# Kernel optimization log

Measured on AMD Instinct MI355X. Metric: run time of the kernel, lower is better.

Reference implementation:

```python
import jax, jax.numpy as jnp
import numpy as np


def setup_inputs() -> dict:
    key = jax.random.key(0)
    k1, k2, k3, k4 = jax.random.split(key, 4)
    B, IN, OUT, S = 8192, 2048, 3072, 8
    scale = 1.0 / (IN ** 0.5)
    x = jax.random.normal(k1, (B, IN), dtype=jnp.float32)
    subject_ids = jax.random.randint(k2, (B,), 0, S, dtype=jnp.int64)
    weights = jax.random.normal(k3, (S, IN, OUT), dtype=jnp.float32) * scale
    bias = jax.random.normal(k4, (S, OUT), dtype=jnp.float32) * scale
    return {"x": x, "subject_ids": subject_ids, "weights": weights, "bias": bias}


def reference(x, subject_ids, weights, bias):
    # Math: out[b] = x[b] @ weights[subject_ids[b]] + bias[subject_ids[b]]
    # Avoid materializing the [B, in, out] gathered weight tensor:
    # contract via a one-hot subject selector instead (same math).
    S = weights.shape[0]
    onehot = jax.nn.one_hot(subject_ids, S, dtype=x.dtype)  # [B, S]
    # [B,d] x [S,d,o] x [B,S] -> [B,o]; intermediate is at most [B,S,o]
    out = jnp.einsum('bd,sdo,bs->bo', x, weights, onehot)
    out = out + bias[subject_ids]  # [B, out]
    return out
```

## Files before the change

### kernel.cpp

```cpp
#include <hip/hip_runtime.h>
#include <hip/hip_bf16.h>
#include <stdint.h>

#define B_ROWS 8192
#define K_DIM  2048
#define N_DIM  3072
#define S_NUM  8

#define BM 128
#define BN 128
#define BK 32
#define NK (K_DIM / BK)
#define MAX_TILES 72

#define LDA 40
#define LDB 40

typedef __bf16 bf16x8 __attribute__((ext_vector_type(8)));
typedef float  f32x4  __attribute__((ext_vector_type(4)));
typedef unsigned int   u32x4 __attribute__((ext_vector_type(4)));
typedef unsigned short u16x8 __attribute__((ext_vector_type(8)));

#define WS_CNT    0
#define WS_OFFS   256
#define WS_TILES  512
#define WS_TILEM  1024
#define WS_RANK   4096
#define WS_PERM   36864
#define WS_XPERM  262144
#define WS_WT     34603008
#define WS_NEED   135266304ULL

__device__ __forceinline__ unsigned int f2bf_pk(float lo, float hi) {
#if __has_builtin(__builtin_amdgcn_cvt_pk_bf16_f32)
    typedef __bf16 bf16x2_t __attribute__((ext_vector_type(2)));
    bf16x2_t v = __builtin_amdgcn_cvt_pk_bf16_f32(lo, hi);
    return __builtin_bit_cast(unsigned int, v);
#else
    unsigned int a = __builtin_bit_cast(unsigned int, lo);
    unsigned int b = __builtin_bit_cast(unsigned int, hi);
    a += 0x7FFFu + ((a >> 16) & 1u);
    b += 0x7FFFu + ((b >> 16) & 1u);
    return (a >> 16) | (b & 0xFFFF0000u);
#endif
}

__device__ __forceinline__ void gl_lds16(const void* g, void* l) {
    __builtin_amdgcn_global_load_lds(
        (const __attribute__((address_space(1))) void*)g,
        (__attribute__((address_space(3))) void*)l, 16, 0, 0);
}

__global__ void zero_cnt_kernel(int* __restrict__ cnt) {
    if (threadIdx.x < S_NUM) cnt[threadIdx.x] = 0;
}

__global__ void bucket_kernel(const int* __restrict__ ids,
                              int* __restrict__ cnt,
                              unsigned short* __restrict__ perm,
                              int* __restrict__ rank) {
    const int b = blockIdx.x * blockDim.x + threadIdx.x;
    const int lane = threadIdx.x & 63;
    const int s = ids[b];
    #pragma unroll
    for (int sub = 0; sub < S_NUM; ++sub) {
        unsigned long long m = __ballot(s == sub);
        if (s == sub) {
            int prefix = __popcll(m & ((1ull << lane) - 1ull));
            int leader = __ffsll((unsigned long long)m) - 1;
            int base = 0;
            if (lane == leader) base = atomicAdd(&cnt[sub], __popcll(m));
            base = __shfl(base, leader);
            perm[sub * B_ROWS + base + prefix] = (unsigned short)b;
            rank[b] = base + prefix;
        }
    }
}

__global__ void plan_kernel(const int* __restrict__ cnt, int* __restrict__ offs,
                            int* __restrict__ tile_s, int* __restrict__ tile_m) {
    if (threadIdx.x == 0 && blockIdx.x == 0) {
        int t = 0, o = 0;
        for (int s = 0; s < S_NUM; ++s) {
            offs[s] = o; o += cnt[s];
            for (int m0 = 0; m0 < cnt[s]; m0 += BM) {
                tile_s[t] = s; tile_m[t] = m0; ++t;
            }
        }
        for (; t < MAX_TILES; ++t) { tile_s[t] = -1; tile_m[t] = 0; }
    }
}

__global__ void convert_x_kernel(const float* __restrict__ x,
                                 const int* __restrict__ ids,
                                 const int* __restrict__ rank,
                                 const int* __restrict__ offs,
                                 unsigned short* __restrict__ xq) {
    const int b = blockIdx.x;
    const int dst = offs[ids[b]] + rank[b];
    const float* src = x + (size_t)b * K_DIM + threadIdx.x * 8;
    f32x4 v0 = *(const f32x4*)(src + 0);
    f32x4 v1 = *(const f32x4*)(src + 4);
    u32x4 p = { f2bf_pk(v0[0], v0[1]), f2bf_pk(v0[2], v0[3]),
                f2bf_pk(v1[0], v1[1]), f2bf_pk(v1[2], v1[3]) };
    *(u32x4*)(xq + (size_t)dst * K_DIM + threadIdx.x * 8) = p;
}

#define TW_LD 136
__global__ void convert_w_kernel(const float* __restrict__ w,
                                 unsigned short* __restrict__ wt) {
    const int kt = blockIdx.x, nt = blockIdx.y, s = blockIdx.z;
    __shared__ __align__(16) unsigned short lds[32 * TW_LD];

    const int tid = threadIdx.x;
    {
        const int k = tid >> 3;
        const int nseg = tid & 7;
        const float* src = w + ((size_t)s * K_DIM + kt * 32 + k) * N_DIM
                             + nt * 128 + nseg * 16;
        f32x4 v0 = *(const f32x4*)(src + 0);
        f32x4 v1 = *(const f32x4*)(src + 4);
        f32x4 v2 = *(const f32x4*)(src + 8);
        f32x4 v3 = *(const f32x4*)(src + 12);
        u32x4 p0 = { f2bf_pk(v0[0], v0[1]), f2bf_pk(v0[2], v0[3]),
                     f2bf_pk(v1[0], v1[1]), f2bf_pk(v1[2], v1[3]) };
        u32x4 p1 = { f2bf_pk(v2[0], v2[1]), f2bf_pk(v2[2], v2[3]),
                     f2bf_pk(v3[0], v3[1]), f2bf_pk(v3[2], v3[3]) };
        *(u32x4*)&lds[k * TW_LD + nseg * 16 + 0] = p0;
        *(u32x4*)&lds[k * TW_LD + nseg * 16 + 8] = p1;
    }
    __syncthreads();
    {
        const int n = tid >> 1;
        const int half = tid & 1;
        u16x8 o0, o1;
        #pragma unroll
        for (int j = 0; j < 8; ++j) {
            o0[j] = lds[(half * 16 + j) * TW_LD + n];
            o1[j] = lds[(half * 16 + 8 + j) * TW_LD + n];
        }
        unsigned short* dst = wt + ((size_t)s * N_DIM + nt * 128 + n) * K_DIM
                                 + kt * 32 + half * 16;
        *(u16x8*)(dst + 0) = o0;
        *(u16x8*)(dst + 8) = o1;
    }
}

__global__ __launch_bounds__(256, 4)
void gemm_bf16_kernel(const unsigned short* __restrict__ xq,
                      const unsigned short* __restrict__ wt,
                      const float* __restrict__ bias,
                      const int* __restrict__ cnt,
                      const int* __restrict__ offs,
                      const int* __restrict__ tile_s,
                      const int* __restrict__ tile_m,
                      const unsigned short* __restrict__ perm,
                      float* __restrict__ out) {
    const int s = tile_s[blockIdx.x];
    if (s < 0) return;
    const int row0 = tile_m[blockIdx.x];
    const int rows = min(BM, cnt[s] - row0);
    const int n0   = blockIdx.y * BN;

    __shared__ __align__(16) unsigned short sA[BM * BK];
    __shared__ __align__(16) unsigned short sB[BN * BK];
    __shared__ int prow[BM];

    const int tid = threadIdx.x;
    if (tid < BM) {
        int rr = (tid < rows) ? tid : (rows - 1);
        prow[tid] = (int)perm[s * B_ROWS + row0 + rr];
    }

    const int lane = tid & 63;
    const int wid  = tid >> 6;
    const int rsub = lane >> 2;
    const int seg  = lane & 3;

    const unsigned short* ag0 = xq + ((size_t)(offs[s] + row0 + wid * 32 + rsub)) * K_DIM + seg * 8;
    const unsigned short* ag1 = ag0 + (size_t)16 * K_DIM;
    const unsigned short* bg0 = wt + ((size_t)s * N_DIM + n0 + wid * 32 + rsub) * K_DIM + seg * 8;
    const unsigned short* bg1 = bg0 + (size_t)16 * K_DIM;
    unsigned short* al0 = &sA[(wid * 32) * BK];
    unsigned short* al1 = &sA[(wid * 32 + 16) * BK];
    unsigned short* bl0 = &sB[(wid * 32) * BK];
    unsigned short* bl1 = &sB[(wid * 32 + 16) * BK];

    const int wm  = (wid >> 1) * 64;
    const int wn  = (wid & 1) * 64;
    const int l15 = lane & 15;
    const int quad = lane >> 4;

    f32x4 acc[4][4] = {};

    for (int ks = 0; ks < NK; ++ks) {
        gl_lds16(ag0, al0);
        gl_lds16(ag1, al1);
        gl_lds16(bg0, bl0);
        gl_lds16(bg1, bl1);
        __syncthreads();

        bf16x8 af[4], bfr[4];
        #pragma unroll
        for (int mt = 0; mt < 4; ++mt)
            af[mt] = *(const bf16x8*)&sA[(wm + mt * 16 + l15) * BK + quad * 8];
        #pragma unroll
        for (int nt = 0; nt < 4; ++nt)
            bfr[nt] = *(const bf16x8*)&sB[(wn + nt * 16 + l15) * BK + quad * 8];

        #pragma unroll
        for (int mt = 0; mt < 4; ++mt)
            #pragma unroll
            for (int nt = 0; nt < 4; ++nt)
                acc[mt][nt] = __builtin_amdgcn_mfma_f32_16x16x32_bf16(
                    af[mt], bfr[nt], acc[mt][nt], 0, 0, 0);

        __syncthreads();
        ag0 += BK; ag1 += BK; bg0 += BK; bg1 += BK;
    }

    float bvals[4];
    #pragma unroll
    for (int nt = 0; nt < 4; ++nt)
        bvals[nt] = bias[s * N_DIM + n0 + wn + nt * 16 + l15];

    #pragma unroll
    for (int mt = 0; mt < 4; ++mt) {
        #pragma unroll
        for (int r = 0; r < 4; ++r) {
            int rl = wm + mt * 16 + quad * 4 + r;
            if (rl < rows) {
                float* op = out + (size_t)prow[rl] * N_DIM + n0 + wn + l15;
                #pragma unroll
                for (int nt = 0; nt < 4; ++nt)
                    op[nt * 16] = acc[mt][nt][r] + bvals[nt];
            }
        }
    }
}

__global__ __launch_bounds__(256, 3)
void subject_gemm_fb(const float* __restrict__ x,
                     const float* __restrict__ w,
                     const float* __restrict__ bias,
                     const int* __restrict__ cnt,
                     const int* __restrict__ tile_s,
                     const int* __restrict__ tile_m,
                     const unsigned short* __restrict__ perm,
                     float* __restrict__ out) {
    const int s = tile_s[blockIdx.x];
    if (s < 0) return;
    const int row0 = tile_m[blockIdx.x];
    const int rows = min(BM, cnt[s] - row0);
    const int n0   = blockIdx.y * BN;

    __shared__ __align__(16) unsigned short sA[BM * LDA];
    __shared__ __align__(16) unsigned short sB[BN * LDB];
    __shared__ int prow[BM];

    const int tid = threadIdx.x;
    if (tid < BM) {
        int rr = (tid < rows) ? tid : (rows - 1);
        prow[tid] = (int)perm[s * B_ROWS + row0 + rr];
    }
    __syncthreads();

    const int ar = tid >> 1;
    const int ah = tid & 1;
    const float* xp = x + (size_t)prow[ar] * K_DIM + ah * 16;
    const int bn  = tid & 127;
    const int bk2 = tid >> 7;
    const float* wp = w + (size_t)s * ((size_t)K_DIM * N_DIM)
                        + (size_t)(bk2 * 16) * N_DIM + (n0 + bn);

    const int lane = tid & 63;
    const int wid  = tid >> 6;
    const int wm   = (wid >> 1) * 64;
    const int wn   = (wid & 1) * 64;
    const int l15  = lane & 15;
    const int quad = lane >> 4;

    f32x4 acc[4][4] = {};
    f32x4 a0, a1, a2, a3;
    float bv[16];
    {
        a0 = *(const f32x4*)(xp + 0);  a1 = *(const f32x4*)(xp + 4);
        a2 = *(const f32x4*)(xp + 8);  a3 = *(const f32x4*)(xp + 12);
        #pragma unroll
        for (int i = 0; i < 16; ++i) bv[i] = wp[(size_t)i * N_DIM];
    }

    for (int ks = 0; ks < NK; ++ks) {
        u32x4 pa0 = { f2bf_pk(a0[0],a0[1]), f2bf_pk(a0[2],a0[3]),
                      f2bf_pk(a1[0],a1[1]), f2bf_pk(a1[2],a1[3]) };
        u32x4 pa1 = { f2bf_pk(a2[0],a2[1]), f2bf_pk(a2[2],a2[3]),
                      f2bf_pk(a3[0],a3[1]), f2bf_pk(a3[2],a3[3]) };
        u32x4 pb0 = { f2bf_pk(bv[0],bv[1]),   f2bf_pk(bv[2],bv[3]),
                      f2bf_pk(bv[4],bv[5]),   f2bf_pk(bv[6],bv[7]) };
        u32x4 pb1 = { f2bf_pk(bv[8],bv[9]),   f2bf_pk(bv[10],bv[11]),
                      f2bf_pk(bv[12],bv[13]), f2bf_pk(bv[14],bv[15]) };

        __syncthreads();
        *(u32x4*)&sA[ar * LDA + ah * 16 + 0] = pa0;
        *(u32x4*)&sA[ar * LDA + ah * 16 + 8] = pa1;
        *(u32x4*)&sB[bn * LDB + bk2 * 16 + 0] = pb0;
        *(u32x4*)&sB[bn * LDB + bk2 * 16 + 8] = pb1;
        __syncthreads();

        if (ks + 1 < NK) {
            const float* xq2 = xp + (ks + 1) * BK;
            a0 = *(const f32x4*)(xq2 + 0);  a1 = *(const f32x4*)(xq2 + 4);
            a2 = *(const f32x4*)(xq2 + 8);  a3 = *(const f32x4*)(xq2 + 12);
            const float* wq = wp + (size_t)((ks + 1) * BK) * N_DIM;
            #pragma unroll
            for (int i = 0; i < 16; ++i) bv[i] = wq[(size_t)i * N_DIM];
        }

        bf16x8 af[4], bfr[4];
        #pragma unroll
        for (int mt = 0; mt < 4; ++mt)
            af[mt] = *(const bf16x8*)&sA[(wm + mt * 16 + l15) * LDA + quad * 8];
        #pragma unroll
        for (int nt = 0; nt < 4; ++nt)
            bfr[nt] = *(const bf16x8*)&sB[(wn + nt * 16 + l15) * LDB + quad * 8];

        #pragma unroll
        for (int mt = 0; mt < 4; ++mt)
            #pragma unroll
            for (int nt = 0; nt < 4; ++nt)
                acc[mt][nt] = __builtin_amdgcn_mfma_f32_16x16x32_bf16(
                    af[mt], bfr[nt], acc[mt][nt], 0, 0, 0);
    }

    float bvals[4];
    #pragma unroll
    for (int nt = 0; nt < 4; ++nt)
        bvals[nt] = bias[s * N_DIM + n0 + wn + nt * 16 + l15];
    #pragma unroll
    for (int mt = 0; mt < 4; ++mt) {
        #pragma unroll
        for (int r = 0; r < 4; ++r) {
            int rl = wm + mt * 16 + quad * 4 + r;
            if (rl < rows) {
                float* op = out + (size_t)prow[rl] * N_DIM + n0 + wn + l15;
                #pragma unroll
                for (int nt = 0; nt < 4; ++nt)
                    op[nt * 16] = acc[mt][nt][r] + bvals[nt];
            }
        }
    }
}

extern "C" void kernel_launch(void* const* d_in, const int* in_sizes, int n_in,
                              void* d_out, int out_size, void* d_ws, size_t ws_size,
                              hipStream_t stream) {
    const float* x    = (const float*)d_in[0];
    const int*   sid  = (const int*)d_in[1];
    const float* w    = (const float*)d_in[2];
    const float* bias = (const float*)d_in[3];
    float* out = (float*)d_out;

    char* ws = (char*)d_ws;
    int* cnt    = (int*)(ws + WS_CNT);
    int* offs   = (int*)(ws + WS_OFFS);
    int* tile_s = (int*)(ws + WS_TILES);
    int* tile_m = (int*)(ws + WS_TILEM);
    int* rank   = (int*)(ws + WS_RANK);
    unsigned short* perm = (unsigned short*)(ws + WS_PERM);

    hipLaunchKernelGGL(zero_cnt_kernel, dim3(1), dim3(64), 0, stream, cnt);
    hipLaunchKernelGGL(bucket_kernel, dim3(B_ROWS / 256), dim3(256), 0, stream,
                       sid, cnt, perm, rank);
    hipLaunchKernelGGL(plan_kernel, dim3(1), dim3(64), 0, stream,
                       cnt, offs, tile_s, tile_m);

    if (ws_size >= WS_NEED) {
        unsigned short* xq = (unsigned short*)(ws + WS_XPERM);
        unsigned short* wt = (unsigned short*)(ws + WS_WT);
        hipLaunchKernelGGL(convert_x_kernel, dim3(B_ROWS), dim3(256), 0, stream,
                           x, sid, rank, offs, xq);
        hipLaunchKernelGGL(convert_w_kernel, dim3(K_DIM / 32, N_DIM / 128, S_NUM),
                           dim3(256), 0, stream, w, wt);
        dim3 grid(MAX_TILES, N_DIM / BN);
        hipLaunchKernelGGL(gemm_bf16_kernel, grid, dim3(256), 0, stream,
                           xq, wt, bias, cnt, offs, tile_s, tile_m, perm, out);
    } else {
        dim3 grid(MAX_TILES, N_DIM / BN);
        hipLaunchKernelGGL(subject_gemm_fb, grid, dim3(256), 0, stream,
                           x, w, bias, cnt, tile_s, tile_m, perm, out);
    }
}
```

Measured before the change: 556.3 us.

## Replace bf16 GEMM with 256x256 double-buffered, XOR-swizzled, ping-pong scheduled kernel

```diff
diff --git a/kernel.cpp b/kernel.cpp
--- a/kernel.cpp
+++ b/kernel.cpp
@@ -7,12 +7,17 @@
 #define N_DIM  3072
 #define S_NUM  8
 
-#define BM 128
-#define BN 128
-#define BK 32
-#define NK (K_DIM / BK)
+#define BM 256
+#define BN 256
+#define BK 64
+#define NT (K_DIM / BK)
+#define MAX_T256 40
+
+#define BMF 128
+#define BNF 128
+#define BKF 32
+#define NKF (K_DIM / BKF)
 #define MAX_TILES 72
-
 #define LDA 40
 #define LDB 40
 
@@ -23,13 +28,15 @@
 
 #define WS_CNT    0
 #define WS_OFFS   256
-#define WS_TILES  512
-#define WS_TILEM  1024
+#define WS_T256S  512
+#define WS_T256M  768
+#define WS_TILES  1024
+#define WS_TILEM  1536
 #define WS_RANK   4096
 #define WS_PERM   36864
 #define WS_XPERM  262144
-#define WS_WT     34603008
-#define WS_NEED   135266304ULL
+#define WS_WT     34865152
+#define WS_NEED   135528448ULL
 
 __device__ __forceinline__ unsigned int f2bf_pk(float lo, float hi) {
 #if __has_builtin(__builtin_amdgcn_cvt_pk_bf16_f32)
@@ -78,16 +85,17 @@
 }
 
 __global__ void plan_kernel(const int* __restrict__ cnt, int* __restrict__ offs,
-                            int* __restrict__ tile_s, int* __restrict__ tile_m) {
+                            int* __restrict__ t256s, int* __restrict__ t256m,
+                            int* __restrict__ tfs, int* __restrict__ tfm) {
     if (threadIdx.x == 0 && blockIdx.x == 0) {
-        int t = 0, o = 0;
+        int t = 0, tf = 0, o = 0;
         for (int s = 0; s < S_NUM; ++s) {
             offs[s] = o; o += cnt[s];
-            for (int m0 = 0; m0 < cnt[s]; m0 += BM) {
-                tile_s[t] = s; tile_m[t] = m0; ++t;
-            }
-        }
-        for (; t < MAX_TILES; ++t) { tile_s[t] = -1; tile_m[t] = 0; }
+            for (int m0 = 0; m0 < cnt[s]; m0 += BM)  { t256s[t] = s; t256m[t] = m0; ++t; }
+            for (int m0 = 0; m0 < cnt[s]; m0 += BMF) { tfs[tf] = s;  tfm[tf] = m0;  ++tf; }
+        }
+        for (; t < MAX_T256; ++t)    { t256s[t] = -1; t256m[t] = 0; }
+        for (; tf < MAX_TILES; ++tf) { tfs[tf]  = -1; tfm[tf]  = 0; }
     }
 }
 
@@ -146,25 +154,24 @@
     }
 }
 
-__global__ __launch_bounds__(256, 4)
-void gemm_bf16_kernel(const unsigned short* __restrict__ xq,
-                      const unsigned short* __restrict__ wt,
-                      const float* __restrict__ bias,
-                      const int* __restrict__ cnt,
-                      const int* __restrict__ offs,
-                      const int* __restrict__ tile_s,
-                      const int* __restrict__ tile_m,
-                      const unsigned short* __restrict__ perm,
-                      float* __restrict__ out) {
+__global__ __launch_bounds__(512, 2)
+void gemm256_kernel(const unsigned short* __restrict__ xq,
+                    const unsigned short* __restrict__ wt,
+                    const float* __restrict__ bias,
+                    const int* __restrict__ cnt,
+                    const int* __restrict__ offs,
+                    const int* __restrict__ tile_s,
+                    const int* __restrict__ tile_m,
+                    const unsigned short* __restrict__ perm,
+                    float* __restrict__ out) {
     const int s = tile_s[blockIdx.x];
     if (s < 0) return;
     const int row0 = tile_m[blockIdx.x];
     const int rows = min(BM, cnt[s] - row0);
     const int n0   = blockIdx.y * BN;
 
-    __shared__ __align__(16) unsigned short sA[BM * BK];
-    __shared__ __align__(16) unsigned short sB[BN * BK];
-    __shared__ int prow[BM];
+    __shared__ __align__(16) char smem[131072 + 1024];
+    int* prow = (int*)(smem + 131072);
 
     const int tid = threadIdx.x;
     if (tid < BM) {
@@ -173,64 +180,128 @@
     }
 
     const int lane = tid & 63;
-    const int wid  = tid >> 6;
-    const int rsub = lane >> 2;
-    const int seg  = lane & 3;
-
-    const unsigned short* ag0 = xq + ((size_t)(offs[s] + row0 + wid * 32 + rsub)) * K_DIM + seg * 8;
-    const unsigned short* ag1 = ag0 + (size_t)16 * K_DIM;
-    const unsigned short* bg0 = wt + ((size_t)s * N_DIM + n0 + wid * 32 + rsub) * K_DIM + seg * 8;
-    const unsigned short* bg1 = bg0 + (size_t)16 * K_DIM;
-    unsigned short* al0 = &sA[(wid * 32) * BK];
-    unsigned short* al1 = &sA[(wid * 32 + 16) * BK];
-    unsigned short* bl0 = &sB[(wid * 32) * BK];
-    unsigned short* bl1 = &sB[(wid * 32 + 16) * BK];
-
-    const int wm  = (wid >> 1) * 64;
-    const int wn  = (wid & 1) * 64;
-    const int l15 = lane & 15;
+    const int w    = tid >> 6;
+    const int wr   = w >> 2;
+    const int wc   = w & 3;
+    const int l15  = lane & 15;
     const int quad = lane >> 4;
 
-    f32x4 acc[4][4] = {};
-
-    for (int ks = 0; ks < NK; ++ks) {
-        gl_lds16(ag0, al0);
-        gl_lds16(ag1, al1);
-        gl_lds16(bg0, bl0);
-        gl_lds16(bg1, bl1);
-        __syncthreads();
-
-        bf16x8 af[4], bfr[4];
-        #pragma unroll
-        for (int mt = 0; mt < 4; ++mt)
-            af[mt] = *(const bf16x8*)&sA[(wm + mt * 16 + l15) * BK + quad * 8];
-        #pragma unroll
-        for (int nt = 0; nt < 4; ++nt)
-            bfr[nt] = *(const bf16x8*)&sB[(wn + nt * 16 + l15) * BK + quad * 8];
-
-        #pragma unroll
-        for (int mt = 0; mt < 4; ++mt)
+    const int srow  = w * 8 + (lane >> 3);
+    const int sperm = ((lane & 7) ^ (lane >> 3)) << 3;
+    const int rowA0 = offs[s] + row0;
+    const unsigned short* aSrc = xq + (size_t)(rowA0 + srow) * K_DIM + sperm;
+    const unsigned short* bSrc = wt + ((size_t)s * N_DIM + n0 + srow) * K_DIM + sperm;
+    char* const aDst = smem + w * 1024;
+    char* const bDst = smem + 65536 + w * 1024;
+
+    auto stageA = [&](int half, int tt, int bb) {
+        int ttc = (tt < NT) ? tt : (NT - 1);
+        const unsigned short* g = aSrc + (size_t)half * (128 * K_DIM) + ttc * BK;
+        char* d = aDst + (bb * 2 + half) * 16384;
+        gl_lds16(g, d);
+        gl_lds16(g + 64 * K_DIM, d + 8192);
+    };
+    auto stageB = [&](int half, int tt, int bb) {
+        int ttc = (tt < NT) ? tt : (NT - 1);
+        const unsigned short* g = bSrc + (size_t)half * (128 * K_DIM) + ttc * BK;
+        char* d = bDst + (bb * 2 + half) * 16384;
+        gl_lds16(g, d);
+        gl_lds16(g + 64 * K_DIM, d + 8192);
+    };
+
+    bf16x8 af[4][2], bfr[2][2];
+    auto ldsA = [&](int mh, int bb) {
+        const char* base = smem + (bb * 2 + wr) * 16384;
+        #pragma unroll
+        for (int mt = 0; mt < 4; ++mt) {
+            const int row = mh * 64 + mt * 16 + l15;
             #pragma unroll
-            for (int nt = 0; nt < 4; ++nt)
-                acc[mt][nt] = __builtin_amdgcn_mfma_f32_16x16x32_bf16(
-                    af[mt], bfr[nt], acc[mt][nt], 0, 0, 0);
-
-        __syncthreads();
-        ag0 += BK; ag1 += BK; bg0 += BK; bg1 += BK;
-    }
+            for (int kk = 0; kk < 2; ++kk) {
+                const int kb = ((kk * 4 + quad) ^ (l15 & 7)) << 4;
+                af[mt][kk] = *(const bf16x8*)(base + row * 128 + kb);
+            }
+        }
+    };
+    auto ldsB = [&](int nh, int bb) {
+        const char* base = smem + 65536 + (bb * 2 + (wc >> 1)) * 16384;
+        #pragma unroll
+        for (int nt = 0; nt < 2; ++nt) {
+            const int row = (wc & 1) * 64 + nh * 32 + nt * 16 + l15;
+            #pragma unroll
+            for (int kk = 0; kk < 2; ++kk) {
+                const int kb = ((kk * 4 + quad) ^ (l15 & 7)) << 4;
+                bfr[nt][kk] = *(const bf16x8*)(base + row * 128 + kb);
+            }
+        }
+    };
+
+    f32x4 acc[8][4] = {};
+    auto mmac = [&](int mh, int nh) {
+        #pragma unroll
+        for (int kk = 0; kk < 2; ++kk)
+            #pragma unroll
+            for (int mt = 0; mt < 4; ++mt)
+                #pragma unroll
+                for (int nt = 0; nt < 2; ++nt)
+                    acc[mh * 4 + mt][nh * 2 + nt] =
+                        __builtin_amdgcn_mfma_f32_16x16x32_bf16(
+                            af[mt][kk], bfr[nt][kk],
+                            acc[mh * 4 + mt][nh * 2 + nt], 0, 0, 0);
+    };
+
+    stageA(0, 0, 0); stageA(1, 0, 0);
+    stageB(0, 0, 0); stageB(1, 0, 0);
+    stageB(0, 1, 1);
+    asm volatile("s_waitcnt vmcnt(2)" ::: "memory");
+    __builtin_amdgcn_s_barrier();
+
+    for (int T = 0; T < NT; ++T) {
+        const int bb = T & 1, nb = bb ^ 1;
+        ldsA(0, bb); ldsB(0, bb);
+        stageB(1, T + 1, nb);
+        __builtin_amdgcn_s_barrier();
+        __builtin_amdgcn_s_setprio(1);
+        mmac(0, 0);
+        __builtin_amdgcn_s_setprio(0);
+        __builtin_amdgcn_s_barrier();
+        ldsA(1, bb);
+        stageA(0, T + 1, nb);
+        __builtin_amdgcn_s_barrier();
+        __builtin_amdgcn_s_setprio(1);
+        mmac(1, 0);
+        __builtin_amdgcn_s_setprio(0);
+        __builtin_amdgcn_s_barrier();
+        ldsB(1, bb);
+        stageA(1, T + 1, nb);
+        __builtin_amdgcn_s_barrier();
+        __builtin_amdgcn_s_setprio(1);
+        mmac(1, 1);
+        __builtin_amdgcn_s_setprio(0);
+        __builtin_amdgcn_s_barrier();
+        ldsA(0, bb);
+        stageB(0, T + 2, bb);
+        asm volatile("s_waitcnt vmcnt(2)" ::: "memory");
+        __builtin_amdgcn_s_barrier();
+        __builtin_amdgcn_s_setprio(1);
+        mmac(0, 1);
+        __builtin_amdgcn_s_setprio(0);
+        __builtin_amdgcn_s_barrier();
+    }
+
+    asm volatile("s_waitcnt vmcnt(0)" ::: "memory");
 
     float bvals[4];
     #pragma unroll
     for (int nt = 0; nt < 4; ++nt)
-        bvals[nt] = bias[s * N_DIM + n0 + wn + nt * 16 + l15];
+        bvals[nt] = bias[s * N_DIM + n0 + wc * 64 + nt * 16 + l15];
 
     #pragma unroll
-    for (int mt = 0; mt < 4; ++mt) {
+    for (int mt = 0; mt < 8; ++mt) {
         #pragma unroll
         for (int r = 0; r < 4; ++r) {
-            int rl = wm + mt * 16 + quad * 4 + r;
+            const int rl = wr * 128 + mt * 16 + quad * 4 + r;
             if (rl < rows) {
-                float* op = out + (size_t)prow[rl] * N_DIM + n0 + wn + l15;
+                float* op = out + (size_t)prow[rl] * N_DIM + n0 + wc * 64 + l15;
                 #pragma unroll
                 for (int nt = 0; nt < 4; ++nt)
                     op[nt * 16] = acc[mt][nt][r] + bvals[nt];
@@ -251,15 +322,15 @@
     const int s = tile_s[blockIdx.x];
     if (s < 0) return;
     const int row0 = tile_m[blockIdx.x];
-    const int rows = min(BM, cnt[s] - row0);
-    const int n0   = blockIdx.y * BN;
-
-    __shared__ __align__(16) unsigned short sA[BM * LDA];
-    __shared__ __align__(16) unsigned short sB[BN * LDB];
-    __shared__ int prow[BM];
+    const int rows = min(BMF, cnt[s] - row0);
+    const int n0   = blockIdx.y * BNF;
+
+    __shared__ __align__(16) unsigned short sA[BMF * LDA];
+    __shared__ __align__(16) unsigned short sB[BNF * LDB];
+    __shared__ int prow[BMF];
 
     const int tid = threadIdx.x;
-    if (tid < BM) {
+    if (tid < BMF) {
         int rr = (tid < rows) ? tid : (rows - 1);
         prow[tid] = (int)perm[s * B_ROWS + row0 + rr];
     }
@@ -290,7 +361,7 @@
         for (int i = 0; i < 16; ++i) bv[i] = wp[(size_t)i * N_DIM];
     }
 
-    for (int ks = 0; ks < NK; ++ks) {
+    for (int ks = 0; ks < NKF; ++ks) {
         u32x4 pa0 = { f2bf_pk(a0[0],a0[1]), f2bf_pk(a0[2],a0[3]),
                       f2bf_pk(a1[0],a1[1]), f2bf_pk(a1[2],a1[3]) };
         u32x4 pa1 = { f2bf_pk(a2[0],a2[1]), f2bf_pk(a2[2],a2[3]),
@@ -307,11 +378,11 @@
         *(u32x4*)&sB[bn * LDB + bk2 * 16 + 8] = pb1;
         __syncthreads();
 
-        if (ks + 1 < NK) {
-            const float* xq2 = xp + (ks + 1) * BK;
+        if (ks + 1 < NKF) {
+            const float* xq2 = xp + (ks + 1) * BKF;
             a0 = *(const f32x4*)(xq2 + 0);  a1 = *(const f32x4*)(xq2 + 4);
             a2 = *(const f32x4*)(xq2 + 8);  a3 = *(const f32x4*)(xq2 + 12);
-            const float* wq = wp + (size_t)((ks + 1) * BK) * N_DIM;
+            const float* wq = wp + (size_t)((ks + 1) * BKF) * N_DIM;
             #pragma unroll
             for (int i = 0; i < 16; ++i) bv[i] = wq[(size_t)i * N_DIM];
         }
@@ -363,8 +434,10 @@
     char* ws = (char*)d_ws;
     int* cnt    = (int*)(ws + WS_CNT);
     int* offs   = (int*)(ws + WS_OFFS);
-    int* tile_s = (int*)(ws + WS_TILES);
-    int* tile_m = (int*)(ws + WS_TILEM);
+    int* t256s  = (int*)(ws + WS_T256S);
+    int* t256m  = (int*)(ws + WS_T256M);
+    int* tfs    = (int*)(ws + WS_TILES);
+    int* tfm    = (int*)(ws + WS_TILEM);
     int* rank   = (int*)(ws + WS_RANK);
     unsigned short* perm = (unsigned short*)(ws + WS_PERM);
 
@@ -372,7 +445,7 @@
     hipLaunchKernelGGL(bucket_kernel, dim3(B_ROWS / 256), dim3(256), 0, stream,
                        sid, cnt, perm, rank);
     hipLaunchKernelGGL(plan_kernel, dim3(1), dim3(64), 0, stream,
-                       cnt, offs, tile_s, tile_m);
+                       cnt, offs, t256s, t256m, tfs, tfm);
 
     if (ws_size >= WS_NEED) {
         unsigned short* xq = (unsigned short*)(ws + WS_XPERM);
@@ -381,12 +454,12 @@
                            x, sid, rank, offs, xq);
         hipLaunchKernelGGL(convert_w_kernel, dim3(K_DIM / 32, N_DIM / 128, S_NUM),
                            dim3(256), 0, stream, w, wt);
-        dim3 grid(MAX_TILES, N_DIM / BN);
-        hipLaunchKernelGGL(gemm_bf16_kernel, grid, dim3(256), 0, stream,
-                           xq, wt, bias, cnt, offs, tile_s, tile_m, perm, out);
+        dim3 grid(MAX_T256, N_DIM / BN);
+        hipLaunchKernelGGL(gemm256_kernel, grid, dim3(512), 0, stream,
+                           xq, wt, bias, cnt, offs, t256s, t256m, perm, out);
     } else {
-        dim3 grid(MAX_TILES, N_DIM / BN);
+        dim3 grid(MAX_TILES, N_DIM / BNF);
         hipLaunchKernelGGL(subject_gemm_fb, grid, dim3(256), 0, stream,
-                           x, w, bias, cnt, tile_s, tile_m, perm, out);
-    }
-}
+                           x, w, bias, cnt, tfs, tfm, perm, out);
+    }
+}
```

After: 519.6 us. 6.6% less time.
